# Kernel tuning notes

Measured on AMD Instinct MI355X. Metric: run time of the kernel, lower is better.

The kernel has to match this reference:

```python
import jax, jax.numpy as jnp
import numpy as np

B, D, N = 256, 256, 100000
NUM_CLUSTERS, NUM_CLASSES = 100, 1000


def setup_inputs() -> dict:
    key = jax.random.key(0)
    k1, k2, k3, k4, k5, k6 = jax.random.split(key, 6)
    return {
        "feature": jax.random.normal(k1, (B, D), dtype=jnp.float32),
        "feature_bank": jax.random.normal(k2, (N, D), dtype=jnp.float32),
        "cluster_label_bank": jax.random.randint(k3, (N,), 0, NUM_CLUSTERS, dtype=jnp.int64)
            if jax.config.jax_enable_x64 else jax.random.randint(k3, (N,), 0, NUM_CLUSTERS).astype(jnp.int32),
        "class_label_bank": jax.random.randint(k4, (N,), 0, NUM_CLASSES).astype(jnp.int32),
        "cluster_idx": jax.random.randint(k5, (B,), 0, NUM_CLUSTERS).astype(jnp.int32),
        "gt_label": jax.random.randint(k6, (B,), 0, NUM_CLASSES).astype(jnp.int32),
    }


def reference(feature, feature_bank, cluster_label_bank, class_label_bank, cluster_idx, gt_label):
    # Masks: primary = same cluster AND different class; fallback = different class only.
    cluster_label_bank = cluster_label_bank.astype(jnp.int32)
    same_cluster = cluster_label_bank[None, :] == cluster_idx[:, None].astype(jnp.int32)  # [B, N]
    diff_class = class_label_bank[None, :] != gt_label[:, None]                            # [B, N]
    mask_primary = same_cluster & diff_class
    has_primary = mask_primary.any(axis=1, keepdims=True)
    mask = jnp.where(has_primary, mask_primary, diff_class)  # [B, N]

    # Euclidean distances (torch.cdist p=2): ||a-b|| via expanded squared form.
    a2 = jnp.sum(feature * feature, axis=1)[:, None]              # [B, 1]
    b2 = jnp.sum(feature_bank * feature_bank, axis=1)[None, :]    # [1, N]
    d2 = a2 + b2 - 2.0 * (feature @ feature_bank.T)               # [B, N]
    dist = jnp.sqrt(jnp.maximum(d2, 0.0))

    # Masked argmin over the bank, then gather negatives.
    dist_masked = jnp.where(mask, dist, jnp.inf)
    neg_idx = jnp.argmin(dist_masked, axis=1)                     # [B]
    negatives = feature_bank[neg_idx]                             # [B, D]
    return negatives
```

## Files before the change

kernel.cpp:

```cpp
#include <hip/hip_runtime.h>
#include <climits>

typedef __attribute__((ext_vector_type(8))) short s8;
typedef __attribute__((ext_vector_type(4))) float f32x4;

#define BQ    256
#define DDIM  256
#define NBANK 100000
#define BN    64
#define NJB   ((NBANK + BN - 1) / BN)
#define SENT  1e30f

__device__ inline void splitElem(float x, s8& h, s8& l, int i) {
    unsigned u  = __float_as_uint(x);
    unsigned uh = (u + 0x8000u) & 0xFFFF0000u;
    h[i] = (short)(uh >> 16);
    float lf = x - __uint_as_float(uh);
    l[i] = (short)((__float_as_uint(lf) + 0x8000u) >> 16);
}

__device__ inline void split8(const float4 v0, const float4 v1, s8& h, s8& l) {
    splitElem(v0.x, h, l, 0); splitElem(v0.y, h, l, 1);
    splitElem(v0.z, h, l, 2); splitElem(v0.w, h, l, 3);
    splitElem(v1.x, h, l, 4); splitElem(v1.y, h, l, 5);
    splitElem(v1.z, h, l, 6); splitElem(v1.w, h, l, 7);
}

__device__ inline float sq8(const float4 v0, const float4 v1, float s) {
    s = fmaf(v0.x, v0.x, s); s = fmaf(v0.y, v0.y, s);
    s = fmaf(v0.z, v0.z, s); s = fmaf(v0.w, v0.w, s);
    s = fmaf(v1.x, v1.x, s); s = fmaf(v1.y, v1.y, s);
    s = fmaf(v1.z, v1.z, s); s = fmaf(v1.w, v1.w, s);
    return s;
}

__global__ __launch_bounds__(512) void split_feature(
    const float* __restrict__ feature, s8* __restrict__ fH, s8* __restrict__ fL)
{
    const int t    = blockIdx.x * 512 + threadIdx.x;
    const int lane = t & 63, ks = (t >> 6) & 7, rt = t >> 9;
    const int row  = rt * 16 + (lane & 15);
    const int k0   = ks * 32 + (lane >> 4) * 8;
    const float* p = feature + (size_t)row * DDIM + k0;
    const float4 v0 = *(const float4*)p;
    const float4 v1 = *(const float4*)(p + 4);
    s8 h, l;
    split8(v0, v1, h, l);
    fH[t] = h; fL[t] = l;
}

__global__ __launch_bounds__(512, 4) void gemm_argmin_msplit(
    const s8* __restrict__ fH, const s8* __restrict__ fL,
    const float* __restrict__ bank,
    const int* __restrict__ cluster_label, const int* __restrict__ class_label,
    const int* __restrict__ cluster_idx,  const int* __restrict__ gt_label,
    float* __restrict__ wsPV, int* __restrict__ wsPI,
    float* __restrict__ wsDV, int* __restrict__ wsDI)
{
    __shared__ __align__(16) s8 bHs[4 * 4 * 64];
    __shared__ __align__(16) s8 bLs[4 * 4 * 64];
    __shared__ float b2s[BN];
    __shared__ int clsS[BN], cluS[BN], rowGt[128], rowClu[128];

    const int tid = threadIdx.x;
    const int bb  = blockIdx.x;
    const int jb  = bb >> 1, mh = bb & 1;
    const int j0  = jb * BN;
    const int r0  = mh * 128;

    const int col = tid >> 3, q = tid & 7;
    const int ct_s = col >> 4, cl_s = col & 15;
    const int sl_s = q >> 1, p_s = q & 1;
    const int w = tid >> 6, lane = tid & 63;
    const int g = lane >> 4, c = lane & 15;

    int jcol = j0 + col; if (jcol >= NBANK) jcol = NBANK - 1;
    const float* gb = bank + (size_t)jcol * DDIM + q * 16;

    if (tid < 128) {
        rowGt[tid]  = gt_label[r0 + tid];
        rowClu[tid] = cluster_idx[r0 + tid];
    }
    if (tid < BN) {
        int jg = j0 + tid; int jc = jg < NBANK ? jg : NBANK - 1;
        clsS[tid] = class_label[jc];
        cluS[tid] = cluster_label[jc];
    }
    float4 a0 = *(const float4*)(gb);
    float4 a1 = *(const float4*)(gb + 4);
    float4 a2 = *(const float4*)(gb + 8);
    float4 a3 = *(const float4*)(gb + 12);

    float sqa = 0.f;
    {
        s8 h, l;
        split8(a0, a1, h, l);
        sqa = sq8(a0, a1, sqa);
        int wi = (((sl_s * 4 + ct_s) * 64 + (p_s * 2 + 0) * 16 + cl_s)) ^ q;
        bHs[wi] = h; bLs[wi] = l;
        split8(a2, a3, h, l);
        sqa = sq8(a2, a3, sqa);
        wi = (((sl_s * 4 + ct_s) * 64 + (p_s * 2 + 1) * 16 + cl_s)) ^ q;
        bHs[wi] = h; bLs[wi] = l;
    }
    __syncthreads();

    a0 = *(const float4*)(gb + 128);
    a1 = *(const float4*)(gb + 132);
    a2 = *(const float4*)(gb + 136);
    a3 = *(const float4*)(gb + 140);

    f32x4 acc[4];
    #pragma unroll
    for (int ct = 0; ct < 4; ++ct)
        acc[ct] = (f32x4){0.f, 0.f, 0.f, 0.f};

    const int RT = mh * 8 + w;

    #pragma unroll
    for (int sl = 0; sl < 4; ++sl) {
        const s8 aH = fH[(RT * 8 + sl) * 64 + lane];
        const s8 aL = fL[(RT * 8 + sl) * 64 + lane];
        const int rx = sl * 2 + (lane >> 5);
        #pragma unroll
        for (int ct = 0; ct < 4; ++ct) {
            const s8 bh = bHs[((sl * 4 + ct) * 64 + lane) ^ rx];
            const s8 bl = bLs[((sl * 4 + ct) * 64 + lane) ^ rx];
            acc[ct] = __builtin_amdgcn_mfma_f32_16x16x32_bf16(aH, bh, acc[ct], 0, 0, 0);
            acc[ct] = __builtin_amdgcn_mfma_f32_16x16x32_bf16(aH, bl, acc[ct], 0, 0, 0);
            acc[ct] = __builtin_amdgcn_mfma_f32_16x16x32_bf16(aL, bh, acc[ct], 0, 0, 0);
            acc[ct] = __builtin_amdgcn_mfma_f32_16x16x32_bf16(aL, bl, acc[ct], 0, 0, 0);
        }
    }
    __syncthreads();

    {
        s8 h, l;
        split8(a0, a1, h, l);
        sqa = sq8(a0, a1, sqa);
        int wi = (((sl_s * 4 + ct_s) * 64 + (p_s * 2 + 0) * 16 + cl_s)) ^ q;
        bHs[wi] = h; bLs[wi] = l;
        split8(a2, a3, h, l);
        sqa = sq8(a2, a3, sqa);
        wi = (((sl_s * 4 + ct_s) * 64 + (p_s * 2 + 1) * 16 + cl_s)) ^ q;
        bHs[wi] = h; bLs[wi] = l;
    }
    sqa += __shfl_xor(sqa, 1);
    sqa += __shfl_xor(sqa, 2);
    sqa += __shfl_xor(sqa, 4);
    if (q == 0) b2s[col] = sqa;
    __syncthreads();

    #pragma unroll
    for (int sl = 0; sl < 4; ++sl) {
        const s8 aH = fH[(RT * 8 + 4 + sl) * 64 + lane];
        const s8 aL = fL[(RT * 8 + 4 + sl) * 64 + lane];
        const int rx = sl * 2 + (lane >> 5);
        #pragma unroll
        for (int ct = 0; ct < 4; ++ct) {
            const s8 bh = bHs[((sl * 4 + ct) * 64 + lane) ^ rx];
            const s8 bl = bLs[((sl * 4 + ct) * 64 + lane) ^ rx];
            acc[ct] = __builtin_amdgcn_mfma_f32_16x16x32_bf16(aH, bh, acc[ct], 0, 0, 0);
            acc[ct] = __builtin_amdgcn_mfma_f32_16x16x32_bf16(aH, bl, acc[ct], 0, 0, 0);
            acc[ct] = __builtin_amdgcn_mfma_f32_16x16x32_bf16(aL, bh, acc[ct], 0, 0, 0);
            acc[ct] = __builtin_amdgcn_mfma_f32_16x16x32_bf16(aL, bl, acc[ct], 0, 0, 0);
        }
    }

    #pragma unroll
    for (int r = 0; r < 4; ++r) {
        const int lrow = w * 16 + g * 4 + r;
        const int myGt = rowGt[lrow], myClu = rowClu[lrow];
        float bpv = SENT, bdv = SENT;
        int   bpi = INT_MAX, bdi = INT_MAX;
        #pragma unroll
        for (int ct = 0; ct < 4; ++ct) {
            const int jg = j0 + ct * 16 + c;
            const float sc = b2s[ct * 16 + c] - 2.f * acc[ct][r];
            if (jg < NBANK && clsS[ct * 16 + c] != myGt) {
                if (sc < bdv) { bdv = sc; bdi = jg; }
                if (cluS[ct * 16 + c] == myClu && sc < bpv) { bpv = sc; bpi = jg; }
            }
        }
        #pragma unroll
        for (int off = 1; off < 16; off <<= 1) {
            float vv = __shfl_xor(bpv, off); int ii = __shfl_xor(bpi, off);
            if (vv < bpv || (vv == bpv && ii < bpi)) { bpv = vv; bpi = ii; }
            vv = __shfl_xor(bdv, off); ii = __shfl_xor(bdi, off);
            if (vv < bdv || (vv == bdv && ii < bdi)) { bdv = vv; bdi = ii; }
        }
        if (c == 0) {
            const size_t o = (size_t)jb * BQ + r0 + lrow;
            wsPV[o] = bpv; wsPI[o] = bpi;
            wsDV[o] = bdv; wsDI[o] = bdi;
        }
    }
}

__global__ __launch_bounds__(256) void reduce_gather(
    const float* __restrict__ wsPV, const int* __restrict__ wsPI,
    const float* __restrict__ wsDV, const int* __restrict__ wsDI,
    const float* __restrict__ bank, float* __restrict__ out)
{
    const int row = blockIdx.x, tid = threadIdx.x;
    float bpv = SENT, bdv = SENT;
    int   bpi = INT_MAX, bdi = INT_MAX;
    for (int b = tid; b < NJB; b += 256) {
        const size_t o = (size_t)b * BQ + row;
        float v = wsPV[o]; int ix = wsPI[o];
        if (v < bpv || (v == bpv && ix < bpi)) { bpv = v; bpi = ix; }
        v = wsDV[o]; ix = wsDI[o];
        if (v < bdv || (v == bdv && ix < bdi)) { bdv = v; bdi = ix; }
    }
    #pragma unroll
    for (int off = 32; off > 0; off >>= 1) {
        float v = __shfl_down(bpv, off); int ix = __shfl_down(bpi, off);
        if (v < bpv || (v == bpv && ix < bpi)) { bpv = v; bpi = ix; }
        v = __shfl_down(bdv, off); ix = __shfl_down(bdi, off);
        if (v < bdv || (v == bdv && ix < bdi)) { bdv = v; bdi = ix; }
    }
    __shared__ float swPV[4], swDV[4];
    __shared__ int   swPI[4], swDI[4];
    __shared__ int   sIdx;
    const int lane = tid & 63, wv = tid >> 6;
    if (lane == 0) { swPV[wv] = bpv; swPI[wv] = bpi; swDV[wv] = bdv; swDI[wv] = bdi; }
    __syncthreads();
    if (tid == 0) {
        float pv = swPV[0]; int pi = swPI[0];
        float dv = swDV[0]; int di = swDI[0];
        #pragma unroll
        for (int w = 1; w < 4; ++w) {
            if (swPV[w] < pv || (swPV[w] == pv && swPI[w] < pi)) { pv = swPV[w]; pi = swPI[w]; }
            if (swDV[w] < dv || (swDV[w] == dv && swDI[w] < di)) { dv = swDV[w]; di = swDI[w]; }
        }
        sIdx = (pi != INT_MAX) ? pi : ((di != INT_MAX) ? di : 0);
    }
    __syncthreads();
    out[row * DDIM + tid] = bank[(size_t)sIdx * DDIM + tid];
}

extern "C" void kernel_launch(void* const* d_in, const int* in_sizes, int n_in,
                              void* d_out, int out_size, void* d_ws, size_t ws_size,
                              hipStream_t stream) {
    const float* feature       = (const float*)d_in[0];
    const float* bank          = (const float*)d_in[1];
    const int*   cluster_label = (const int*)d_in[2];
    const int*   class_label   = (const int*)d_in[3];
    const int*   cluster_idx   = (const int*)d_in[4];
    const int*   gt_label      = (const int*)d_in[5];
    float* out = (float*)d_out;

    s8* fH = (s8*)d_ws;
    s8* fL = fH + 8192;
    float* base = (float*)((char*)d_ws + 2 * 8192 * sizeof(s8));
    const size_t per = (size_t)BQ * NJB;
    float* wsPV = base;
    int*   wsPI = (int*)base + per;
    float* wsDV = base + 2 * per;
    int*   wsDI = (int*)base + 3 * per;

    hipLaunchKernelGGL(split_feature, dim3(16), dim3(512), 0, stream, feature, fH, fL);
    hipLaunchKernelGGL(gemm_argmin_msplit, dim3(NJB * 2), dim3(512), 0, stream,
                       fH, fL, bank, cluster_label, class_label, cluster_idx, gt_label,
                       wsPV, wsPI, wsDV, wsDI);
    hipLaunchKernelGGL(reduce_gather, dim3(BQ), dim3(256), 0, stream,
                       wsPV, wsPI, wsDV, wsDI, bank, out);
}
```

Baseline: 230.1 us.

## Drop low-low MFMA term and replace partial-result reduce with packed atomicMin

Removes the aL*bL bf16 MFMA from the split-precision GEMM, using three products instead of four. Replaces the per-block workspace of partial argmins and its separate reduction kernel with 64-bit atomicMin on packed (order-preserving float key, index) values, initialized in the split kernel. Raises wave priority around the MFMA loops. This trades a small precision loss and atomic contention on 512 addresses for less matrix work and workspace traffic.

```diff
diff --git a/kernel.cpp b/kernel.cpp
--- a/kernel.cpp
+++ b/kernel.cpp
@@ -34,10 +34,17 @@
     return s;
 }
 
-__global__ __launch_bounds__(512) void split_feature(
-    const float* __restrict__ feature, s8* __restrict__ fH, s8* __restrict__ fL)
+__device__ inline unsigned fkey(float f) {
+    unsigned u = __float_as_uint(f);
+    return u ^ (((int)u < 0) ? 0xFFFFFFFFu : 0x80000000u);
+}
+
+__global__ __launch_bounds__(512) void split_feature_init(
+    const float* __restrict__ feature, s8* __restrict__ fH, s8* __restrict__ fL,
+    unsigned long long* __restrict__ mins)
 {
     const int t    = blockIdx.x * 512 + threadIdx.x;
+    if (blockIdx.x == 0) mins[threadIdx.x] = ~0ull;
     const int lane = t & 63, ks = (t >> 6) & 7, rt = t >> 9;
     const int row  = rt * 16 + (lane & 15);
     const int k0   = ks * 32 + (lane >> 4) * 8;
@@ -54,8 +61,7 @@
     const float* __restrict__ bank,
     const int* __restrict__ cluster_label, const int* __restrict__ class_label,
     const int* __restrict__ cluster_idx,  const int* __restrict__ gt_label,
-    float* __restrict__ wsPV, int* __restrict__ wsPI,
-    float* __restrict__ wsDV, int* __restrict__ wsDI)
+    unsigned long long* __restrict__ mins)
 {
     __shared__ __align__(16) s8 bHs[4 * 4 * 64];
     __shared__ __align__(16) s8 bLs[4 * 4 * 64];
@@ -117,6 +123,7 @@
 
     const int RT = mh * 8 + w;
 
+    __builtin_amdgcn_s_setprio(1);
     #pragma unroll
     for (int sl = 0; sl < 4; ++sl) {
         const s8 aH = fH[(RT * 8 + sl) * 64 + lane];
@@ -129,9 +136,9 @@
             acc[ct] = __builtin_amdgcn_mfma_f32_16x16x32_bf16(aH, bh, acc[ct], 0, 0, 0);
             acc[ct] = __builtin_amdgcn_mfma_f32_16x16x32_bf16(aH, bl, acc[ct], 0, 0, 0);
             acc[ct] = __builtin_amdgcn_mfma_f32_16x16x32_bf16(aL, bh, acc[ct], 0, 0, 0);
-            acc[ct] = __builtin_amdgcn_mfma_f32_16x16x32_bf16(aL, bl, acc[ct], 0, 0, 0);
-        }
-    }
+        }
+    }
+    __builtin_amdgcn_s_setprio(0);
     __syncthreads();
 
     {
@@ -151,6 +158,7 @@
     if (q == 0) b2s[col] = sqa;
     __syncthreads();
 
+    __builtin_amdgcn_s_setprio(1);
     #pragma unroll
     for (int sl = 0; sl < 4; ++sl) {
         const s8 aH = fH[(RT * 8 + 4 + sl) * 64 + lane];
@@ -163,9 +171,9 @@
             acc[ct] = __builtin_amdgcn_mfma_f32_16x16x32_bf16(aH, bh, acc[ct], 0, 0, 0);
             acc[ct] = __builtin_amdgcn_mfma_f32_16x16x32_bf16(aH, bl, acc[ct], 0, 0, 0);
             acc[ct] = __builtin_amdgcn_mfma_f32_16x16x32_bf16(aL, bh, acc[ct], 0, 0, 0);
-            acc[ct] = __builtin_amdgcn_mfma_f32_16x16x32_bf16(aL, bl, acc[ct], 0, 0, 0);
-        }
-    }
+        }
+    }
+    __builtin_amdgcn_s_setprio(0);
 
     #pragma unroll
     for (int r = 0; r < 4; ++r) {
@@ -190,53 +198,32 @@
             if (vv < bdv || (vv == bdv && ii < bdi)) { bdv = vv; bdi = ii; }
         }
         if (c == 0) {
-            const size_t o = (size_t)jb * BQ + r0 + lrow;
-            wsPV[o] = bpv; wsPI[o] = bpi;
-            wsDV[o] = bdv; wsDI[o] = bdi;
-        }
-    }
-}
-
-__global__ __launch_bounds__(256) void reduce_gather(
-    const float* __restrict__ wsPV, const int* __restrict__ wsPI,
-    const float* __restrict__ wsDV, const int* __restrict__ wsDI,
+            const int grow = r0 + lrow;
+            if (bpv < SENT)
+                atomicMin(&mins[grow],
+                          ((unsigned long long)fkey(bpv) << 32) | (unsigned)bpi);
+            if (bdv < SENT)
+                atomicMin(&mins[256 + grow],
+                          ((unsigned long long)fkey(bdv) << 32) | (unsigned)bdi);
+        }
+    }
+}
+
+__global__ __launch_bounds__(256) void gather_out(
+    const unsigned long long* __restrict__ mins,
     const float* __restrict__ bank, float* __restrict__ out)
 {
     const int row = blockIdx.x, tid = threadIdx.x;
-    float bpv = SENT, bdv = SENT;
-    int   bpi = INT_MAX, bdi = INT_MAX;
-    for (int b = tid; b < NJB; b += 256) {
-        const size_t o = (size_t)b * BQ + row;
-        float v = wsPV[o]; int ix = wsPI[o];
-        if (v < bpv || (v == bpv && ix < bpi)) { bpv = v; bpi = ix; }
-        v = wsDV[o]; ix = wsDI[o];
-        if (v < bdv || (v == bdv && ix < bdi)) { bdv = v; bdi = ix; }
-    }
-    #pragma unroll
-    for (int off = 32; off > 0; off >>= 1) {
-        float v = __shfl_down(bpv, off); int ix = __shfl_down(bpi, off);
-        if (v < bpv || (v == bpv && ix < bpi)) { bpv = v; bpi = ix; }
-        v = __shfl_down(bdv, off); ix = __shfl_down(bdi, off);
-        if (v < bdv || (v == bdv && ix < bdi)) { bdv = v; bdi = ix; }
-    }
-    __shared__ float swPV[4], swDV[4];
-    __shared__ int   swPI[4], swDI[4];
-    __shared__ int   sIdx;
-    const int lane = tid & 63, wv = tid >> 6;
-    if (lane == 0) { swPV[wv] = bpv; swPI[wv] = bpi; swDV[wv] = bdv; swDI[wv] = bdi; }
-    __syncthreads();
+    __shared__ int sIdx;
     if (tid == 0) {
-        float pv = swPV[0]; int pi = swPI[0];
-        float dv = swDV[0]; int di = swDI[0];
-        #pragma unroll
-        for (int w = 1; w < 4; ++w) {
-            if (swPV[w] < pv || (swPV[w] == pv && swPI[w] < pi)) { pv = swPV[w]; pi = swPI[w]; }
-            if (swDV[w] < dv || (swDV[w] == dv && swDI[w] < di)) { dv = swDV[w]; di = swDI[w]; }
-        }
-        sIdx = (pi != INT_MAX) ? pi : ((di != INT_MAX) ? di : 0);
-    }
-    __syncthreads();
-    out[row * DDIM + tid] = bank[(size_t)sIdx * DDIM + tid];
+        unsigned long long p = mins[row], d = mins[256 + row];
+        int idx = 0;
+        if (p != ~0ull)      idx = (int)(p & 0xFFFFFFFFull);
+        else if (d != ~0ull) idx = (int)(d & 0xFFFFFFFFull);
+        sIdx = idx;
+    }
+    __syncthreads();
+    out[(size_t)row * DDIM + tid] = bank[(size_t)sIdx * DDIM + tid];
 }
 
 extern "C" void kernel_launch(void* const* d_in, const int* in_sizes, int n_in,
@@ -252,17 +239,13 @@
 
     s8* fH = (s8*)d_ws;
     s8* fL = fH + 8192;
-    float* base = (float*)((char*)d_ws + 2 * 8192 * sizeof(s8));
-    const size_t per = (size_t)BQ * NJB;
-    float* wsPV = base;
-    int*   wsPI = (int*)base + per;
-    float* wsDV = base + 2 * per;
-    int*   wsDI = (int*)base + 3 * per;
-
-    hipLaunchKernelGGL(split_feature, dim3(16), dim3(512), 0, stream, feature, fH, fL);
+    unsigned long long* mins = (unsigned long long*)((char*)d_ws + 2 * 8192 * sizeof(s8));
+
+    hipLaunchKernelGGL(split_feature_init, dim3(16), dim3(512), 0, stream,
+                       feature, fH, fL, mins);
     hipLaunchKernelGGL(gemm_argmin_msplit, dim3(NJB * 2), dim3(512), 0, stream,
                        fH, fL, bank, cluster_label, class_label, cluster_idx, gt_label,
-                       wsPV, wsPI, wsDV, wsDI);
-    hipLaunchKernelGGL(reduce_gather, dim3(BQ), dim3(256), 0, stream,
-                       wsPV, wsPI, wsDV, wsDI, bank, out);
-}
+                       mins);
+    hipLaunchKernelGGL(gather_out, dim3(BQ), dim3(256), 0, stream,
+                       mins, bank, out);
+}
```

Result: slower. 272.2 us (+18.3%).
